# Kernel tuning notes

Measured on AMD Instinct MI355X. Metric: run time of the kernel, lower is better.

The kernel has to match this reference:

```python
import jax, jax.numpy as jnp
import numpy as np

BOX_W, CLS_W, OBJ_W = 0.05, 0.5, 1.0


def setup_inputs() -> dict:
    key = jax.random.key(0)
    k1, k2, k3 = jax.random.split(key, 3)
    predictions = jax.random.normal(k1, (16, 3, 160, 160, 9), dtype=jnp.float32)
    coords = jax.random.uniform(k2, (16, 32, 4), dtype=jnp.float32)  # xy, wh in [0,1)
    cls = jax.random.randint(k3, (16, 32, 1), 0, 4).astype(jnp.float32)
    targets = jnp.concatenate([cls, coords], axis=-1)  # [B, T, 5]: class, x, y, w, h
    return {"predictions": predictions, "targets": targets}


def _loss(predictions, targets):
    B = predictions.shape[0]
    D = predictions.shape[-1]
    T = targets.shape[1]

    def per_image(pred, tgt):
        pred = pred.reshape(-1, D)                 # [P, D]
        pxy, pwh = pred[:, :2], pred[:, 2:4]
        pobj, pcls = pred[:, 4], pred[:, 5:]
        txy, twh = tgt[:, 1:3], tgt[:, 3:5]
        tcls = tgt[:, 0].astype(jnp.int32)
        # pairwise IoU [P, T]
        p1, p2 = pxy - pwh / 2, pxy + pwh / 2
        t1, t2 = txy - twh / 2, txy + twh / 2
        lo = jnp.maximum(p1[:, None, :], t1[None, :, :])
        hi = jnp.minimum(p2[:, None, :], t2[None, :, :])
        inter = jnp.prod(jnp.clip(hi - lo, 0.0), axis=-1)
        pa = jnp.prod(p2 - p1, axis=-1)[:, None]
        ta = jnp.prod(t2 - t1, axis=-1)[None, :]
        iou = (inter / (pa + ta - inter + 1e-6)).max(axis=1)   # [P]
        pos = iou > 0.5
        neg = iou < 0.3
        posf = pos.astype(pred.dtype)
        negf = neg.astype(pred.dtype)
        npos = posf.sum()
        nneg = negf.sum()
        # k-th positive prediction pairs with target[k mod T] (torch .repeat semantics)
        rank = jnp.cumsum(pos.astype(jnp.int32)) - 1
        tidx = jnp.maximum(rank, 0) % T
        # box: MSE over positive pred_xy vs tiled target_xy (mean over elems)
        sq = (pxy - txy[tidx]) ** 2                # [P, 2]
        box = jnp.where(npos > 0, (sq * posf[:, None]).sum() / (2.0 * npos), 0.0)
        # cls: cross entropy over positives
        logp = jax.nn.log_softmax(pcls, axis=-1)
        ce = -jnp.take_along_axis(logp, tcls[tidx][:, None], axis=-1)[:, 0]
        cls = jnp.where(npos > 0, (ce * posf).sum() / npos, 0.0)
        # obj: BCE-with-logits, target 1 on positives, 0 on negatives
        obj = jnp.where(npos > 0, (jax.nn.softplus(-pobj) * posf).sum() / npos, 0.0) \
            + jnp.where(nneg > 0, (jax.nn.softplus(pobj) * negf).sum() / nneg, 0.0)
        return box, cls, obj

    box, cls, obj = jax.vmap(per_image)(predictions, targets)
    box_loss = box.sum() / B
    cls_loss = cls.sum() / B
    obj_loss = obj.sum() / B
    total = BOX_W * box_loss + CLS_W * cls_loss + OBJ_W * obj_loss
    return total, box_loss, cls_loss, obj_loss


def reference(predictions, targets):
    return _loss(predictions, targets)
```

## Files before the change

### kernel.cpp

```cpp
#include <hip/hip_runtime.h>
#include <cstdint>
#include <cstddef>

constexpr int kB     = 16;
constexpr int kN     = 76800;
constexpr int kD     = 9;
constexpr int kT     = 32;
constexpr int kBlk1  = 256;
constexpr int kApB   = 1024;
constexpr int kNB    = kN / kApB;
constexpr int kWords = kN / 64;

__device__ __forceinline__ float softplusf(float x) {
  return fmaxf(x, 0.f) + log1pf(expf(-fabsf(x)));
}

__global__ __launch_bounds__(kB * kT) void pass0_kernel(
    const float* __restrict__ tgt, float* __restrict__ twork)
{
  const int t = threadIdx.x;
  const int b = t >> 5, j = t & 31;
  const float* tp = tgt + ((size_t)b * kT + j) * 5;
  const float tx = tp[1], ty = tp[2], tw = tp[3], th = tp[4];
  const float t1x = tx - tw * 0.5f, t1y = ty - th * 0.5f;
  const float t2x = tx + tw * 0.5f, t2y = ty + th * 0.5f;
  float* w = twork + (size_t)b * 5 * kT;
  w[0 * kT + j] = t1x;
  w[1 * kT + j] = t1y;
  w[2 * kT + j] = t2x;
  w[3 * kT + j] = t2y;
  w[4 * kT + j] = (t2x - t1x) * (t2y - t1y);
}

__global__ __launch_bounds__(kBlk1) void k1_iou_kernel(
    const float* __restrict__ pred, const float* __restrict__ twork,
    int* __restrict__ cnt, int* __restrict__ nnegA,
    float* __restrict__ objP, float* __restrict__ objN,
    unsigned long long* __restrict__ posBits)
{
  __shared__ float s_red[4][2];
  __shared__ int   s_cnt[4][2];

  const int b    = blockIdx.y;
  const int blk  = blockIdx.x;
  const int tid  = threadIdx.x;
  const int lane = tid & 63;
  const int wv   = tid >> 6;
  const float* tw = twork + (size_t)b * 5 * kT;

  const int a0 = blk * kApB + wv * 256 + 4 * lane;
  const float4* q = reinterpret_cast<const float4*>(
      pred + ((size_t)b * kN + a0) * kD);
  const float4 q0 = q[0], q1 = q[1], q2 = q[2], q3 = q[3];
  const float4 q4 = q[4], q5 = q[5], q6 = q[6], q7 = q[7];

  float px[4], py[4], pw_[4], ph[4], pobj[4];
  px[0]=q0.x; py[0]=q0.y; pw_[0]=q0.z; ph[0]=q0.w; pobj[0]=q1.x;
  px[1]=q2.y; py[1]=q2.z; pw_[1]=q2.w; ph[1]=q3.x; pobj[1]=q3.y;
  px[2]=q4.z; py[2]=q4.w; pw_[2]=q5.x; ph[2]=q5.y; pobj[2]=q5.z;
  px[3]=q6.w; py[3]=q7.x; pw_[3]=q7.y; ph[3]=q7.z; pobj[3]=q7.w;

  float p1x[4], p1y[4], p2x[4], p2y[4], pa[4];
  #pragma unroll
  for (int k = 0; k < 4; ++k) {
    p1x[k] = px[k] - pw_[k] * 0.5f;  p1y[k] = py[k] - ph[k] * 0.5f;
    p2x[k] = px[k] + pw_[k] * 0.5f;  p2y[k] = py[k] + ph[k] * 0.5f;
    pa[k]  = (p2x[k] - p1x[k]) * (p2y[k] - p1y[k]);
  }

  bool posA[4] = {false,false,false,false};
  bool negA[4] = {true,true,true,true};
  #pragma unroll
  for (int j = 0; j < kT; ++j) {
    const float t1x = tw[0 * kT + j];
    const float t1y = tw[1 * kT + j];
    const float t2x = tw[2 * kT + j];
    const float t2y = tw[3 * kT + j];
    const float ta  = tw[4 * kT + j];
    #pragma unroll
    for (int k = 0; k < 4; ++k) {
      const float lox = fmaxf(p1x[k], t1x), loy = fmaxf(p1y[k], t1y);
      const float hix = fminf(p2x[k], t2x), hiy = fminf(p2y[k], t2y);
      const float inter = fmaxf(hix - lox, 0.f) * fmaxf(hiy - loy, 0.f);
      const float d = ((pa[k] + ta) - inter) + 1e-6f;
      posA[k] = posA[k] || ((d >= 0.f) && (inter > 0.5f * d));
      negA[k] = negA[k] && ((d <  0.f) || (inter < 0.3f * d));
    }
  }

  float op = 0.f, on = 0.f;
  int pc = 0, nc = 0;
  const int chunk = blk * 4 + wv;
  #pragma unroll
  for (int k = 0; k < 4; ++k) {
    op += posA[k] ? softplusf(-pobj[k]) : 0.f;
    on += negA[k] ? softplusf( pobj[k]) : 0.f;
    const unsigned long long pm = __ballot(posA[k]);
    const unsigned long long nm = __ballot(negA[k]);
    if (lane == 0)
      posBits[(size_t)b * kWords + chunk * 4 + k] = pm;
    pc += __popcll(pm);
    nc += __popcll(nm);
  }

  #pragma unroll
  for (int off = 32; off > 0; off >>= 1) {
    op += __shfl_down(op, off, 64);
    on += __shfl_down(on, off, 64);
  }
  if (lane == 0) {
    s_red[wv][0] = op;  s_red[wv][1] = on;
    s_cnt[wv][0] = pc;  s_cnt[wv][1] = nc;
  }
  __syncthreads();
  if (tid == 0) {
    float sop = 0.f, son = 0.f; int tpc = 0, tnc = 0;
    #pragma unroll
    for (int w = 0; w < 4; ++w) {
      sop += s_red[w][0]; son += s_red[w][1];
      tpc += s_cnt[w][0]; tnc += s_cnt[w][1];
    }
    const int slot = b * kNB + blk;
    cnt[slot]   = tpc;
    nnegA[slot] = tnc;
    objP[slot]  = sop;
    objN[slot]  = son;
  }
}

__global__ __launch_bounds__(kBlk1) void k2_pos_kernel(
    const float* __restrict__ pred, const float* __restrict__ tgt,
    const int* __restrict__ cnt,
    const unsigned long long* __restrict__ posBits,
    float* __restrict__ p3sq, float* __restrict__ p3ce)
{
  __shared__ float s_tx[kT], s_ty[kT];
  __shared__ int   s_tc[kT];
  __shared__ int   s_ctot[4];
  __shared__ int   s_pre[4];
  __shared__ float s_red[4][2];

  const int b = blockIdx.y, blk = blockIdx.x, tid = threadIdx.x;
  const int slot = b * kNB + blk;
  const int lane = tid & 63, wv = tid >> 6;

  const unsigned long long* wp =
      posBits + (size_t)b * kWords + (blk * 4 + wv) * 4;
  const unsigned long long m0 = wp[0], m1 = wp[1], m2 = wp[2], m3 = wp[3];
  const int ctot = __popcll(m0) + __popcll(m1) + __popcll(m2) + __popcll(m3);
  if (lane == 0) s_ctot[wv] = ctot;

  int c = (tid < blk) ? cnt[b * kNB + tid] : 0;
  #pragma unroll
  for (int off = 32; off > 0; off >>= 1) c += __shfl_down(c, off, 64);
  if (lane == 0) s_pre[wv] = c;

  if (tid < kT) {
    const float* tp = tgt + ((size_t)b * kT + tid) * 5;
    s_tx[tid] = tp[1]; s_ty[tid] = tp[2];
    s_tc[tid] = (int)tp[0];
  }
  __syncthreads();

  int tot = 0, base = 0;
  #pragma unroll
  for (int w = 0; w < 4; ++w) { tot += s_ctot[w]; base += s_pre[w]; }
  if (tot == 0) {
    if (tid == 0) { p3sq[slot] = 0.f; p3ce[slot] = 0.f; }
    return;
  }
  for (int w = 0; w < wv; ++w) base += s_ctot[w];

  const unsigned long long low = ((unsigned long long)1 << lane) - 1ull;
  const int beforeLanes = __popcll(m0 & low) + __popcll(m1 & low)
                        + __popcll(m2 & low) + __popcll(m3 & low);
  const int bit0 = (int)((m0 >> lane) & 1ull);
  const int bit1 = (int)((m1 >> lane) & 1ull);
  const int bit2 = (int)((m2 >> lane) & 1ull);
  const int bit3 = (int)((m3 >> lane) & 1ull);
  const int kbit[4] = {bit0, bit1, bit2, bit3};

  const int a0 = blk * kApB + wv * 256 + 4 * lane;
  float sqc = 0.f, cec = 0.f;
  int prior = 0;
  #pragma unroll
  for (int k = 0; k < 4; ++k) {
    if (kbit[k]) {
      const int ord = base + beforeLanes + prior;
      const int tix = ord & (kT - 1);
      const float* p = pred + ((size_t)b * kN + (a0 + k)) * kD;
      const float dx = p[0] - s_tx[tix];
      const float dy = p[1] - s_ty[tix];
      sqc += dx * dx + dy * dy;
      const float c0 = p[5], c1 = p[6], c2 = p[7], c3 = p[8];
      const float m = fmaxf(fmaxf(c0, c1), fmaxf(c2, c3));
      const float lse = m + logf(expf(c0 - m) + expf(c1 - m) + expf(c2 - m) + expf(c3 - m));
      const int tc = s_tc[tix];
      const float cv = (tc == 0) ? c0 : (tc == 1) ? c1 : (tc == 2) ? c2 : c3;
      cec += lse - cv;
    }
    prior += kbit[k];
  }

  #pragma unroll
  for (int off = 32; off > 0; off >>= 1) {
    sqc += __shfl_down(sqc, off, 64);
    cec += __shfl_down(cec, off, 64);
  }
  if (lane == 0) { s_red[wv][0] = sqc; s_red[wv][1] = cec; }
  __syncthreads();
  if (tid == 0) {
    float ss = 0.f, cs = 0.f;
    #pragma unroll
    for (int w = 0; w < 4; ++w) { ss += s_red[w][0]; cs += s_red[w][1]; }
    p3sq[slot] = ss;
    p3ce[slot] = cs;
  }
}

__global__ __launch_bounds__(256) void k3_final_kernel(
    const int* __restrict__ cnt, const int* __restrict__ nnegA,
    const float* __restrict__ objP, const float* __restrict__ objN,
    const float* __restrict__ p3sq, const float* __restrict__ p3ce,
    float* __restrict__ out)
{
  __shared__ float s_sq[16][17], s_ce[16][17], s_op[16][17], s_on[16][17];
  __shared__ int   s_np[16][17], s_nn[16][17];
  const int tid = threadIdx.x;
  const int b = tid & 15, g = tid >> 4;
  int   np = 0, nn = 0;
  float op = 0.f, on = 0.f, sq = 0.f, ce = 0.f;
  for (int k = g; k < kNB; k += 16) {
    const int s = b * kNB + k;
    np += cnt[s];  nn += nnegA[s];
    op += objP[s]; on += objN[s];
    sq += p3sq[s]; ce += p3ce[s];
  }
  s_np[g][b] = np; s_nn[g][b] = nn;
  s_op[g][b] = op; s_on[g][b] = on;
  s_sq[g][b] = sq; s_ce[g][b] = ce;
  __syncthreads();

  float box = 0.f, cls = 0.f, obj = 0.f;
  if (tid < kB) {
    int tnp = 0, tnn = 0;
    float top = 0.f, ton = 0.f, tsq = 0.f, tce = 0.f;
    #pragma unroll
    for (int gg = 0; gg < 16; ++gg) {
      tnp += s_np[gg][tid]; tnn += s_nn[gg][tid];
      top += s_op[gg][tid]; ton += s_on[gg][tid];
      tsq += s_sq[gg][tid]; tce += s_ce[gg][tid];
    }
    const float np_ = (float)tnp;
    const float nn_ = (float)tnn;
    if (np_ > 0.f) {
      box = tsq / (2.0f * np_);
      cls = tce / np_;
      obj = top / np_;
    }
    if (nn_ > 0.f) obj += ton / nn_;
  }
  #pragma unroll
  for (int off = 8; off > 0; off >>= 1) {
    box += __shfl_down(box, off, 64);
    cls += __shfl_down(cls, off, 64);
    obj += __shfl_down(obj, off, 64);
  }
  if (tid == 0) {
    box *= (1.f / 16.f); cls *= (1.f / 16.f); obj *= (1.f / 16.f);
    out[0] = 0.05f * box + 0.5f * cls + 1.0f * obj;
    out[1] = box;
    out[2] = cls;
    out[3] = obj;
  }
}

extern "C" void kernel_launch(void* const* d_in, const int* in_sizes, int n_in,
                              void* d_out, int out_size, void* d_ws, size_t ws_size,
                              hipStream_t stream)
{
  const float* pred = (const float*)d_in[0];
  const float* tgt  = (const float*)d_in[1];
  float* out = (float*)d_out;

  char* ws = (char*)d_ws;
  float* twork = (float*)(ws);
  int*   cnt   = (int*)(ws + 10240);
  int*   nnegA = (int*)(ws + 15104);
  float* objP  = (float*)(ws + 19968);
  float* objN  = (float*)(ws + 24832);
  unsigned long long* posBits =
      (unsigned long long*)(ws + 29696);
  float* p3sq  = (float*)(ws + 183296);
  float* p3ce  = (float*)(ws + 188160);

  pass0_kernel<<<1, kB * kT, 0, stream>>>(tgt, twork);
  k1_iou_kernel<<<dim3(kNB, kB), kBlk1, 0, stream>>>(
      pred, twork, cnt, nnegA, objP, objN, posBits);
  k2_pos_kernel<<<dim3(kNB, kB), kBlk1, 0, stream>>>(
      pred, tgt, cnt, posBits, p3sq, p3ce);
  k3_final_kernel<<<1, 256, 0, stream>>>(
      cnt, nnegA, objP, objN, p3sq, p3ce, out);
}
```

Before: 115.1 us.

## Fuse four loss kernels into one cooperative kernel with grid syncs

Replaces the four-launch pipeline (target prep, IoU pass, positive-pair pass, final reduce) with a single cooperative kernel. The kernel stages the target boxes in shared memory, processes three tiles per block, and separates the phases with grid-wide syncs. The aim is to remove launch gaps and inter-kernel drains, since the workload is small. In exchange it adds grid barrier cost, runs the final reduce on one block while the others sit idle, and keeps the old multi-kernel path as a fallback if occupancy or the cooperative launch fails.

```diff
diff --git a/kernel.cpp b/kernel.cpp
--- a/kernel.cpp
+++ b/kernel.cpp
@@ -1,18 +1,263 @@
 #include <hip/hip_runtime.h>
+#include <hip/hip_cooperative_groups.h>
 #include <cstdint>
 #include <cstddef>
+
+namespace cg = cooperative_groups;
 
 constexpr int kB     = 16;
 constexpr int kN     = 76800;
 constexpr int kD     = 9;
 constexpr int kT     = 32;
-constexpr int kBlk1  = 256;
+constexpr int kBlk   = 256;
 constexpr int kApB   = 1024;
 constexpr int kNB    = kN / kApB;
+constexpr int kTPB   = 3;
+constexpr int kGX    = kNB / kTPB;
 constexpr int kWords = kN / 64;
+constexpr int kCUs   = 256;
 
 __device__ __forceinline__ float softplusf(float x) {
   return fmaxf(x, 0.f) + log1pf(expf(-fabsf(x)));
+}
+
+__global__ __launch_bounds__(kBlk) void fused_kernel(
+    const float* __restrict__ pred, const float* __restrict__ tgt,
+    int* __restrict__ cnt, int* __restrict__ nnegA,
+    float* __restrict__ objP, float* __restrict__ objN,
+    unsigned long long* __restrict__ posBits,
+    float* __restrict__ p3sq, float* __restrict__ p3ce,
+    float* __restrict__ out)
+{
+  cg::grid_group grid = cg::this_grid();
+
+  __shared__ float s_t1x[kT], s_t1y[kT], s_t2x[kT], s_t2y[kT], s_ta[kT];
+  __shared__ float s_tx[kT], s_ty[kT];
+  __shared__ int   s_tc[kT];
+  __shared__ float s_red[4][2];
+  __shared__ int   s_icnt[4][2];
+  __shared__ int   s_ctot[4], s_pre[4];
+  __shared__ float f3_sq[16][17], f3_ce[16][17], f3_op[16][17], f3_on[16][17];
+  __shared__ int   f3_np[16][17], f3_nn[16][17];
+
+  const int b    = blockIdx.y;
+  const int blk  = blockIdx.x;
+  const int tid  = threadIdx.x;
+  const int lane = tid & 63;
+  const int wv   = tid >> 6;
+
+  if (tid < kT) {
+    const float* tp = tgt + ((size_t)b * kT + tid) * 5;
+    const float tx = tp[1], ty = tp[2], tw = tp[3], th = tp[4];
+    const float t1x = tx - tw * 0.5f, t1y = ty - th * 0.5f;
+    const float t2x = tx + tw * 0.5f, t2y = ty + th * 0.5f;
+    s_t1x[tid] = t1x; s_t1y[tid] = t1y;
+    s_t2x[tid] = t2x; s_t2y[tid] = t2y;
+    s_ta[tid]  = (t2x - t1x) * (t2y - t1y);
+    s_tx[tid] = tx; s_ty[tid] = ty;
+    s_tc[tid] = (int)tp[0];
+  }
+  __syncthreads();
+
+  for (int t = 0; t < kTPB; ++t) {
+    const int tile = blk + kGX * t;
+    const int a0 = tile * kApB + wv * 256 + 4 * lane;
+    const float4* q = reinterpret_cast<const float4*>(
+        pred + ((size_t)b * kN + a0) * kD);
+    const float4 q0 = q[0], q1 = q[1], q2 = q[2], q3 = q[3];
+    const float4 q4 = q[4], q5 = q[5], q6 = q[6], q7 = q[7];
+
+    float px[4], py[4], pw_[4], ph[4], pobj[4];
+    px[0]=q0.x; py[0]=q0.y; pw_[0]=q0.z; ph[0]=q0.w; pobj[0]=q1.x;
+    px[1]=q2.y; py[1]=q2.z; pw_[1]=q2.w; ph[1]=q3.x; pobj[1]=q3.y;
+    px[2]=q4.z; py[2]=q4.w; pw_[2]=q5.x; ph[2]=q5.y; pobj[2]=q5.z;
+    px[3]=q6.w; py[3]=q7.x; pw_[3]=q7.y; ph[3]=q7.z; pobj[3]=q7.w;
+
+    float p1x[4], p1y[4], p2x[4], p2y[4], pa[4];
+    #pragma unroll
+    for (int k = 0; k < 4; ++k) {
+      p1x[k] = px[k] - pw_[k] * 0.5f;  p1y[k] = py[k] - ph[k] * 0.5f;
+      p2x[k] = px[k] + pw_[k] * 0.5f;  p2y[k] = py[k] + ph[k] * 0.5f;
+      pa[k]  = (p2x[k] - p1x[k]) * (p2y[k] - p1y[k]);
+    }
+
+    bool posA[4] = {false,false,false,false};
+    bool negA[4] = {true,true,true,true};
+    #pragma unroll
+    for (int j = 0; j < kT; ++j) {
+      const float t1x = s_t1x[j], t1y = s_t1y[j];
+      const float t2x = s_t2x[j], t2y = s_t2y[j];
+      const float ta  = s_ta[j];
+      #pragma unroll
+      for (int k = 0; k < 4; ++k) {
+        const float lox = fmaxf(p1x[k], t1x), loy = fmaxf(p1y[k], t1y);
+        const float hix = fminf(p2x[k], t2x), hiy = fminf(p2y[k], t2y);
+        const float inter = fmaxf(hix - lox, 0.f) * fmaxf(hiy - loy, 0.f);
+        const float d = ((pa[k] + ta) - inter) + 1e-6f;
+        posA[k] = posA[k] || ((d >= 0.f) && (inter > 0.5f * d));
+        negA[k] = negA[k] && ((d <  0.f) || (inter < 0.3f * d));
+      }
+    }
+
+    float op = 0.f, on = 0.f;
+    int pc = 0, nc = 0;
+    const int chunk = tile * 4 + wv;
+    #pragma unroll
+    for (int k = 0; k < 4; ++k) {
+      op += posA[k] ? softplusf(-pobj[k]) : 0.f;
+      on += negA[k] ? softplusf( pobj[k]) : 0.f;
+      const unsigned long long pm = __ballot(posA[k]);
+      const unsigned long long nm = __ballot(negA[k]);
+      if (lane == 0)
+        posBits[(size_t)b * kWords + chunk * 4 + k] = pm;
+      pc += __popcll(pm);
+      nc += __popcll(nm);
+    }
+
+    #pragma unroll
+    for (int off = 32; off > 0; off >>= 1) {
+      op += __shfl_down(op, off, 64);
+      on += __shfl_down(on, off, 64);
+    }
+    if (lane == 0) {
+      s_red[wv][0] = op;  s_red[wv][1] = on;
+      s_icnt[wv][0] = pc; s_icnt[wv][1] = nc;
+    }
+    __syncthreads();
+    if (tid == 0) {
+      float sop = 0.f, son = 0.f; int tpc = 0, tnc = 0;
+      #pragma unroll
+      for (int w = 0; w < 4; ++w) {
+        sop += s_red[w][0]; son += s_red[w][1];
+        tpc += s_icnt[w][0]; tnc += s_icnt[w][1];
+      }
+      const int slot = b * kNB + tile;
+      cnt[slot]   = tpc;
+      nnegA[slot] = tnc;
+      objP[slot]  = sop;
+      objN[slot]  = son;
+    }
+    __syncthreads();
+  }
+
+  grid.sync();
+
+  for (int t = 0; t < kTPB; ++t) {
+    const int tile = blk + kGX * t;
+    const unsigned long long* wp =
+        posBits + (size_t)b * kWords + (tile * 4 + wv) * 4;
+    const unsigned long long m0 = wp[0], m1 = wp[1], m2 = wp[2], m3 = wp[3];
+    const int ctot = __popcll(m0) + __popcll(m1) + __popcll(m2) + __popcll(m3);
+    if (lane == 0) s_ctot[wv] = ctot;
+
+    int c = (tid < tile) ? cnt[b * kNB + tid] : 0;
+    #pragma unroll
+    for (int off = 32; off > 0; off >>= 1) c += __shfl_down(c, off, 64);
+    if (lane == 0) s_pre[wv] = c;
+    __syncthreads();
+
+    int base = 0;
+    #pragma unroll
+    for (int w = 0; w < 4; ++w) base += s_pre[w];
+    for (int w = 0; w < wv; ++w) base += s_ctot[w];
+
+    const unsigned long long low = ((unsigned long long)1 << lane) - 1ull;
+    const int beforeLanes = __popcll(m0 & low) + __popcll(m1 & low)
+                          + __popcll(m2 & low) + __popcll(m3 & low);
+    const int kbit[4] = { (int)((m0 >> lane) & 1ull), (int)((m1 >> lane) & 1ull),
+                          (int)((m2 >> lane) & 1ull), (int)((m3 >> lane) & 1ull) };
+
+    const int a0 = tile * kApB + wv * 256 + 4 * lane;
+    float sqc = 0.f, cec = 0.f;
+    int prior = 0;
+    #pragma unroll
+    for (int k = 0; k < 4; ++k) {
+      if (kbit[k]) {
+        const int ord = base + beforeLanes + prior;
+        const int tix = ord & (kT - 1);
+        const float* p = pred + ((size_t)b * kN + (a0 + k)) * kD;
+        const float dx = p[0] - s_tx[tix];
+        const float dy = p[1] - s_ty[tix];
+        sqc += dx * dx + dy * dy;
+        const float c0 = p[5], c1 = p[6], c2 = p[7], c3 = p[8];
+        const float m = fmaxf(fmaxf(c0, c1), fmaxf(c2, c3));
+        const float lse = m + logf(expf(c0 - m) + expf(c1 - m)
+                                 + expf(c2 - m) + expf(c3 - m));
+        const int tc = s_tc[tix];
+        const float cv = (tc == 0) ? c0 : (tc == 1) ? c1 : (tc == 2) ? c2 : c3;
+        cec += lse - cv;
+      }
+      prior += kbit[k];
+    }
+
+    #pragma unroll
+    for (int off = 32; off > 0; off >>= 1) {
+      sqc += __shfl_down(sqc, off, 64);
+      cec += __shfl_down(cec, off, 64);
+    }
+    if (lane == 0) { s_red[wv][0] = sqc; s_red[wv][1] = cec; }
+    __syncthreads();
+    if (tid == 0) {
+      float ss = 0.f, cs = 0.f;
+      #pragma unroll
+      for (int w = 0; w < 4; ++w) { ss += s_red[w][0]; cs += s_red[w][1]; }
+      const int slot = b * kNB + tile;
+      p3sq[slot] = ss;
+      p3ce[slot] = cs;
+    }
+    __syncthreads();
+  }
+
+  grid.sync();
+
+  if (blk == 0 && b == 0) {
+    const int ib = tid & 15, g = tid >> 4;
+    int   np = 0, nn = 0;
+    float top_ = 0.f, ton_ = 0.f, sq = 0.f, ce = 0.f;
+    for (int k = g; k < kNB; k += 16) {
+      const int s = ib * kNB + k;
+      np += cnt[s];    nn += nnegA[s];
+      top_ += objP[s]; ton_ += objN[s];
+      sq += p3sq[s];   ce += p3ce[s];
+    }
+    f3_np[g][ib] = np;   f3_nn[g][ib] = nn;
+    f3_op[g][ib] = top_; f3_on[g][ib] = ton_;
+    f3_sq[g][ib] = sq;   f3_ce[g][ib] = ce;
+    __syncthreads();
+
+    float box = 0.f, cls = 0.f, obj = 0.f;
+    if (tid < kB) {
+      int tnp = 0, tnn = 0;
+      float sop = 0.f, son = 0.f, tsq = 0.f, tce = 0.f;
+      #pragma unroll
+      for (int gg = 0; gg < 16; ++gg) {
+        tnp += f3_np[gg][tid]; tnn += f3_nn[gg][tid];
+        sop += f3_op[gg][tid]; son += f3_on[gg][tid];
+        tsq += f3_sq[gg][tid]; tce += f3_ce[gg][tid];
+      }
+      const float np_ = (float)tnp;
+      const float nn_ = (float)tnn;
+      if (np_ > 0.f) {
+        box = tsq / (2.0f * np_);
+        cls = tce / np_;
+        obj = sop / np_;
+      }
+      if (nn_ > 0.f) obj += son / nn_;
+    }
+    #pragma unroll
+    for (int off = 8; off > 0; off >>= 1) {
+      box += __shfl_down(box, off, 64);
+      cls += __shfl_down(cls, off, 64);
+      obj += __shfl_down(obj, off, 64);
+    }
+    if (tid == 0) {
+      box *= (1.f / 16.f); cls *= (1.f / 16.f); obj *= (1.f / 16.f);
+      out[0] = 0.05f * box + 0.5f * cls + 1.0f * obj;
+      out[1] = box;
+      out[2] = cls;
+      out[3] = obj;
+    }
+  }
 }
 
 __global__ __launch_bounds__(kB * kT) void pass0_kernel(
@@ -32,7 +277,7 @@
   w[4 * kT + j] = (t2x - t1x) * (t2y - t1y);
 }
 
-__global__ __launch_bounds__(kBlk1) void k1_iou_kernel(
+__global__ __launch_bounds__(kBlk) void k1_iou_kernel(
     const float* __restrict__ pred, const float* __restrict__ twork,
     int* __restrict__ cnt, int* __restrict__ nnegA,
     float* __restrict__ objP, float* __restrict__ objN,
@@ -72,10 +317,8 @@
   bool negA[4] = {true,true,true,true};
   #pragma unroll
   for (int j = 0; j < kT; ++j) {
-    const float t1x = tw[0 * kT + j];
-    const float t1y = tw[1 * kT + j];
-    const float t2x = tw[2 * kT + j];
-    const float t2y = tw[3 * kT + j];
+    const float t1x = tw[0 * kT + j], t1y = tw[1 * kT + j];
+    const float t2x = tw[2 * kT + j], t2y = tw[3 * kT + j];
     const float ta  = tw[4 * kT + j];
     #pragma unroll
     for (int k = 0; k < 4; ++k) {
@@ -128,7 +371,7 @@
   }
 }
 
-__global__ __launch_bounds__(kBlk1) void k2_pos_kernel(
+__global__ __launch_bounds__(kBlk) void k2_pos_kernel(
     const float* __restrict__ pred, const float* __restrict__ tgt,
     const int* __restrict__ cnt,
     const unsigned long long* __restrict__ posBits,
@@ -174,11 +417,8 @@
   const unsigned long long low = ((unsigned long long)1 << lane) - 1ull;
   const int beforeLanes = __popcll(m0 & low) + __popcll(m1 & low)
                         + __popcll(m2 & low) + __popcll(m3 & low);
-  const int bit0 = (int)((m0 >> lane) & 1ull);
-  const int bit1 = (int)((m1 >> lane) & 1ull);
-  const int bit2 = (int)((m2 >> lane) & 1ull);
-  const int bit3 = (int)((m3 >> lane) & 1ull);
-  const int kbit[4] = {bit0, bit1, bit2, bit3};
+  const int kbit[4] = { (int)((m0 >> lane) & 1ull), (int)((m1 >> lane) & 1ull),
+                        (int)((m2 >> lane) & 1ull), (int)((m3 >> lane) & 1ull) };
 
   const int a0 = blk * kApB + wv * 256 + 4 * lane;
   float sqc = 0.f, cec = 0.f;
@@ -194,7 +434,8 @@
       sqc += dx * dx + dy * dy;
       const float c0 = p[5], c1 = p[6], c2 = p[7], c3 = p[8];
       const float m = fmaxf(fmaxf(c0, c1), fmaxf(c2, c3));
-      const float lse = m + logf(expf(c0 - m) + expf(c1 - m) + expf(c2 - m) + expf(c3 - m));
+      const float lse = m + logf(expf(c0 - m) + expf(c1 - m)
+                               + expf(c2 - m) + expf(c3 - m));
       const int tc = s_tc[tix];
       const float cv = (tc == 0) ? c0 : (tc == 1) ? c1 : (tc == 2) ? c2 : c3;
       cec += lse - cv;
@@ -218,7 +459,7 @@
   }
 }
 
-__global__ __launch_bounds__(256) void k3_final_kernel(
+__global__ __launch_bounds__(kBlk) void k3_final_kernel(
     const int* __restrict__ cnt, const int* __restrict__ nnegA,
     const float* __restrict__ objP, const float* __restrict__ objN,
     const float* __restrict__ p3sq, const float* __restrict__ p3ce,
@@ -284,21 +525,35 @@
   float* out = (float*)d_out;
 
   char* ws = (char*)d_ws;
-  float* twork = (float*)(ws);
-  int*   cnt   = (int*)(ws + 10240);
-  int*   nnegA = (int*)(ws + 15104);
-  float* objP  = (float*)(ws + 19968);
-  float* objN  = (float*)(ws + 24832);
+  int*   cnt   = (int*)(ws);
+  int*   nnegA = (int*)(ws + 4864);
+  float* objP  = (float*)(ws + 9728);
+  float* objN  = (float*)(ws + 14592);
+  float* p3sq  = (float*)(ws + 19456);
+  float* p3ce  = (float*)(ws + 24320);
   unsigned long long* posBits =
-      (unsigned long long*)(ws + 29696);
-  float* p3sq  = (float*)(ws + 183296);
-  float* p3ce  = (float*)(ws + 188160);
+      (unsigned long long*)(ws + 29184);
+  float* twork = (float*)(ws + 182784);
+
+  int maxPerCU = 0;
+  hipError_t qe = hipOccupancyMaxActiveBlocksPerMultiprocessor(
+      &maxPerCU, (const void*)fused_kernel, kBlk, 0);
+  bool coop_ok = (qe == hipSuccess) && (maxPerCU * kCUs >= kGX * kB);
+
+  if (coop_ok) {
+    void* args[] = { (void*)&pred, (void*)&tgt, (void*)&cnt, (void*)&nnegA,
+                     (void*)&objP, (void*)&objN, (void*)&posBits,
+                     (void*)&p3sq, (void*)&p3ce, (void*)&out };
+    hipError_t le = hipLaunchCooperativeKernel(
+        (const void*)fused_kernel, dim3(kGX, kB), dim3(kBlk), args, 0, stream);
+    if (le == hipSuccess) return;
+  }
 
   pass0_kernel<<<1, kB * kT, 0, stream>>>(tgt, twork);
-  k1_iou_kernel<<<dim3(kNB, kB), kBlk1, 0, stream>>>(
+  k1_iou_kernel<<<dim3(kNB, kB), kBlk, 0, stream>>>(
       pred, twork, cnt, nnegA, objP, objN, posBits);
-  k2_pos_kernel<<<dim3(kNB, kB), kBlk1, 0, stream>>>(
+  k2_pos_kernel<<<dim3(kNB, kB), kBlk, 0, stream>>>(
       pred, tgt, cnt, posBits, p3sq, p3ce);
-  k3_final_kernel<<<1, 256, 0, stream>>>(
+  k3_final_kernel<<<1, kBlk, 0, stream>>>(
       cnt, nnegA, objP, objN, p3sq, p3ce, out);
 }
```

Result: no change. 115.6 us (+0.4%).
